# Kernel tuning notes

Measured on AMD Instinct MI355X. Metric: run time of the kernel, lower is better.

## Reference

```python
import jax, jax.numpy as jnp
import numpy as np

NX = 48
NY = 48
K0DX = 0.2026833935483871
N_PML = 8
_PI = 3.1415926


def _fun_s(u):
    # PML stretch factor s(u) = kappa(u) + 1j*sigma_over_omega(u)
    power_kappa = 3
    kappa_max = 15
    power_sigma = 3
    lambda_over_dx = 40
    sigma_over_omega_max = 0.8 * (power_sigma + 1) * lambda_over_dx / (2 * _PI)
    return (1.0 + (kappa_max - 1) * u ** power_kappa) + 1j * (sigma_over_omega_max * u ** power_sigma)


def _lap1d_pml(N, N_L, N_R):
    # 1D second-difference operator with stretched-coordinate PML (dense numpy, constant)
    ddx1 = np.eye(N + 1, N) - np.eye(N + 1, N, k=-1)   # forward difference (N+1, N)
    ddx2 = -ddx1.T                                      # (N, N+1)
    s_half = np.ones(N + 1, dtype=np.complex128)
    s_int = np.ones(N, dtype=np.complex128)
    if N_R > 0:
        s_half[N - N_R:N + 1] = _fun_s(np.arange(0.5, N_R + 1, 1.0) / (N_R + 1))
        s_int[N - N_R:N] = _fun_s(np.arange(1.0, N_R + 1, 1.0) / (N_R + 1))
    if N_L > 0:
        s_half[N_L::-1] = _fun_s(np.arange(0.5, N_L + 1, 1.0) / (N_L + 1))
        s_int[N_L - 1::-1] = _fun_s(np.arange(1.0, N_L + 1, 1.0) / (N_L + 1))
    return np.diag(1.0 / s_int) @ ddx2 @ np.diag(1.0 / s_half) @ ddx1


def _build_A1():
    # 2D Helmholtz Laplacian with PML: kron(Ax, I) + kron(I, Ay), dense 2304x2304 complex64
    Ax = _lap1d_pml(NX, N_PML, N_PML)
    Ay = _lap1d_pml(NY, N_PML, N_PML)
    return (np.kron(Ax, np.eye(NY)) + np.kron(np.eye(NX), Ay)).astype(np.complex64)


_A1 = _build_A1()  # constant system matrix part


def setup_inputs() -> dict:
    key = jax.random.key(0)
    k1, k2, k3, k4, k5 = jax.random.split(key, 5)
    return {
        "n_prediction": jax.random.uniform(k1, (1, NX, NY, 1), dtype=jnp.float32),
        "n_predict_allresults": jax.random.normal(k2, (1, NX, NY, 1), dtype=jnp.float32),
        "x_b": jax.random.normal(k3, (1, NX, NY, 1), dtype=jnp.float32),
        "y_aim": jax.random.normal(k4, (1, NX, NY, 2), dtype=jnp.float32),
        "simulation_region": jax.random.normal(k5, (1, NX, NY, 1), dtype=jnp.float32),
    }


def reference(n_prediction, n_predict_allresults, x_b, y_aim, simulation_region):
    A1 = jnp.asarray(_A1)  # (2304, 2304) complex64
    # A = A1 + k0dx^2 * diag(n^2), with n flattened after [0,2,1,3] transpose
    n_c = n_prediction.astype(jnp.complex64)
    n_flat = jnp.transpose(n_c, (0, 2, 1, 3)).reshape(-1)  # (2304,)
    A = A1 + jnp.diag((K0DX ** 2) * n_flat ** 2)
    # RHS b, same transpose+flatten convention
    b = jnp.transpose(x_b.astype(jnp.complex64), (0, 2, 1, 3)).reshape(NX * NY, 1)
    # Dense complex linear solve A psi = b
    psi = jnp.linalg.solve(A, b).reshape(1, NX, NY, 1)
    psi_tot = jnp.transpose(psi, (0, 2, 1, 3))  # (1, 48, 48, 1) complex64
    y_c = y_aim.astype(jnp.complex64)
    err1 = psi_tot * y_c[:, :, :, 0:1]
    err2 = psi_tot * y_c[:, :, :, 1:2]
    en1 = y_c[:, :, :, 0:1] * y_c[:, :, :, 0:1]
    en2 = y_c[:, :, :, 1:2] * y_c[:, :, :, 1:2]
    return jnp.concatenate([err1, err2, en1, en2], axis=-1)  # (1, 48, 48, 4) complex64
```

## Files before the change

### kernel.cpp

```cpp
#include <hip/hip_runtime.h>


#define NXY 48
#define NN  2304

typedef float2 cplx;
typedef double2 zplx;

__device__ __forceinline__ cplx cmk(float x, float y){ return make_float2(x,y); }
__device__ __forceinline__ cplx cmul(cplx a, cplx b){
    return cmk(fmaf(a.x,b.x,-(a.y*b.y)), fmaf(a.x,b.y, a.y*b.x));
}
__device__ __forceinline__ cplx cadd(cplx a, cplx b){ return cmk(a.x+b.x, a.y+b.y); }
__device__ __forceinline__ cplx csub(cplx a, cplx b){ return cmk(a.x-b.x, a.y-b.y); }
__device__ __forceinline__ cplx cneg(cplx a){ return cmk(-a.x,-a.y); }
__device__ __forceinline__ cplx cfms(cplx c, cplx a, cplx b){
    float re = fmaf(-a.x, b.x, fmaf( a.y, b.y, c.x));
    float im = fmaf(-a.x, b.y, fmaf(-a.y, b.x, c.y));
    return cmk(re, im);
}
__device__ __forceinline__ cplx cfma_(cplx c, cplx a, cplx b){
    float re = fmaf(a.x, b.x, fmaf(-a.y, b.y, c.x));
    float im = fmaf(a.x, b.y, fmaf( a.y, b.x, c.y));
    return cmk(re, im);
}
__device__ __forceinline__ cplx cinv(cplx a){
    float s = 1.0f/fmaf(a.x,a.x, a.y*a.y);
    return cmk(a.x*s, -a.y*s);
}
__device__ __forceinline__ cplx shfl_c(cplx v, int lane){
    return cmk(__shfl(v.x, lane), __shfl(v.y, lane));
}
__device__ __forceinline__ cplx bfly_c(cplx v){
    v.x += __shfl_xor(v.x,1); v.y += __shfl_xor(v.y,1);
    v.x += __shfl_xor(v.x,2); v.y += __shfl_xor(v.y,2);
    v.x += __shfl_xor(v.x,4); v.y += __shfl_xor(v.y,4);
    return v;
}

__device__ __forceinline__ zplx zmul64(zplx a, zplx b){
    return make_double2(a.x*b.x - a.y*b.y, a.x*b.y + a.y*b.x);
}
__device__ __forceinline__ zplx zadd64(zplx a, zplx b){ return make_double2(a.x+b.x, a.y+b.y); }
__device__ __forceinline__ zplx zneg64(zplx a){ return make_double2(-a.x, -a.y); }
__device__ __forceinline__ zplx zinv64(zplx a){
    double s = 1.0/(a.x*a.x + a.y*a.y);
    return make_double2(a.x*s, -a.y*s);
}
__device__ __forceinline__ zplx fun_s(double u){
    const double sig = 0.8*4.0*40.0/(2.0*3.1415926);
    double u3 = u*u*u;
    return make_double2(1.0 + 14.0*u3, sig*u3);
}
__device__ __forceinline__ zplx s_half_at(int j){
    if (j <= 8)  return fun_s((8.5 - (double)j)/9.0);
    if (j >= 40) return fun_s(((double)(j-40) + 0.5)/9.0);
    return make_double2(1.0, 0.0);
}
__device__ __forceinline__ zplx s_int_at(int j){
    if (j <= 7)  return fun_s((8.0 - (double)j)/9.0);
    if (j >= 40) return fun_s(((double)(j-40) + 1.0)/9.0);
    return make_double2(1.0, 0.0);
}

__device__ __forceinline__ void gj48(cplx (&m)[6][6], int lr, int lc){
    #pragma unroll 1
    for (int kr=0; kr<8; ++kr){
        bool prow = (lr==kr), pcol = (lc==kr);
        int rsrc = (kr<<3)|lc;
        int csrc = (lr<<3)|kr;
        int dsrc = (kr<<3)|kr;
        #pragma unroll
        for (int kj=0;kj<6;++kj){
            cplx pv = shfl_c(m[kj][kj], dsrc);
            cplx d  = cinv(pv);
            cplx rs[6], cs[6];
            #pragma unroll
            for (int j=0;j<6;++j) rs[j] = shfl_c(m[kj][j], rsrc);
            #pragma unroll
            for (int i=0;i<6;++i) cs[i] = shfl_c(m[i][kj], csrc);
            cplx rsp[6];
            #pragma unroll
            for (int j=0;j<6;++j) rsp[j] = cmul(d, rs[j]);
            cplx u[6];
            #pragma unroll
            for (int i=0;i<6;++i) u[i] = cs[i];
            if (prow) u[kj] = csub(pv, cmk(1.f,0.f));
            #pragma unroll
            for (int i=0;i<6;++i){
                #pragma unroll
                for (int j=0;j<6;++j) m[i][j] = cfms(m[i][j], u[i], rsp[j]);
            }
            if (pcol){
                #pragma unroll
                for (int i=0;i<6;++i) m[i][kj] = cneg(cmul(d, cs[i]));
                if (prow) m[kj][kj] = d;
            }
        }
    }
}

__global__ __launch_bounds__(128,1) void helm_babe(
    const float* __restrict__ n_pred,
    const float* __restrict__ xb,
    const float* __restrict__ yaim,
    float*       __restrict__ out,
    int                       out_size,
    float2*      __restrict__ wsG)
{
    __shared__ cplx dgv[NXY], lov[NXY], hiv[NXY];
    __shared__ float nk[NN];
    __shared__ float bb[NN];
    __shared__ cplx zv[NN];
    __shared__ cplx Hx[NN];
    __shared__ cplx vv[NXY];

    const int t    = threadIdx.x;
    const int lane = t & 63;
    const int wid  = t >> 6;
    const int lr = lane>>3, lc = lane&7;
    const int r0 = 6*lr, c0v = 6*lc;
    const int diagl = (lc<<3)|lc;
    const double k2 = 0.2026833935483871*0.2026833935483871;

    if (t < NXY){
        int a = t;
        zplx isha  = zinv64(s_half_at(a));
        zplx isha1 = zinv64(s_half_at(a+1));
        zplx isi   = zinv64(s_int_at(a));
        zplx dgd = zneg64(zmul64(isi, zadd64(isha,isha1)));
        zplx lod = zmul64(isi, isha);
        zplx hid = zmul64(isi, isha1);
        dgv[a] = cmk((float)dgd.x,(float)dgd.y);
        lov[a] = cmk((float)lod.x,(float)lod.y);
        hiv[a] = cmk((float)hid.x,(float)hid.y);
    }
    for (int e=t; e<NN; e+=128){
        int i_=e/48, a_=e%48;
        float nv = n_pred[a_*48+i_];
        nk[e] = (float)(k2*(double)nv*(double)nv);
        bb[e] = xb[a_*48+i_];
    }
    __syncthreads();

    const int dir    = (wid==0) ? 1 : -1;
    const int ibeg   = (wid==0) ? 0 : 47;
    const int nsteps = (wid==0) ? 25 : 23;

    cplx g[6][6];
    cplx m[6][6];
    cplx zrow[6];
    #pragma unroll
    for (int i=0;i<6;++i) zrow[i] = cmk(0.f,0.f);

    #pragma unroll 1
    for (int step=0; step<nsteps; ++step){
        int ib = ibeg + dir*step;
        bool full = !(wid==0 && step==24);

        cplx zc[6];
        #pragma unroll
        for (int j=0;j<6;++j) zc[j] = shfl_c(zrow[j], diagl);

        cplx ci = cmk(0.f,0.f), czp = cmk(0.f,0.f);
        if (step>0){
            if (dir>0){ ci = cmul(lov[ib], hiv[ib-1]); czp = lov[ib]; }
            else      { ci = cmul(hiv[ib], lov[ib+1]); czp = hiv[ib]; }
        }
        bool same  = (lc==lr), rightn = (lc==lr+1), leftn = (lc+1==lr);
        cplx p[6];
        #pragma unroll
        for (int i=0;i<6;++i){
            int r = r0+i;
            cplx dgr = dgv[r], lor = lov[r], hir = hiv[r];
            cplx ddi = cadd(cadd(dgv[ib], dgr), cmk(nk[ib*48+r],0.f));
            cplx acc = cmk(0.f,0.f);
            #pragma unroll
            for (int j=0;j<6;++j){
                cplx v = (step>0)? cneg(cmul(ci, g[i][j])) : cmk(0.f,0.f);
                if (same){
                    if (j==i)   v = cadd(v, ddi);
                    if (j==i+1) v = cadd(v, hir);
                    if (j+1==i) v = cadd(v, lor);
                }
                if (rightn && i==5 && j==0) v = cadd(v, hir);
                if (leftn  && i==0 && j==5) v = cadd(v, lor);
                m[i][j] = v;
                if (step>0) acc = cfma_(acc, g[i][j], zc[j]);
            }
            p[i] = acc;
        }
        if (step>0){
            #pragma unroll
            for (int i=0;i<6;++i){
                cplx w = bfly_c(p[i]);
                zrow[i] = cfms(cmk(bb[ib*48+r0+i],0.f), czp, w);
            }
        } else {
            #pragma unroll
            for (int i=0;i<6;++i) zrow[i] = cmk(bb[ib*48+r0+i], 0.f);
        }
        if (lc==0){
            #pragma unroll
            for (int i=0;i<6;++i) zv[ib*48+r0+i] = zrow[i];
        }

        if (full){
            gj48(m, lr, lc);
            if (ib == 25){
                #pragma unroll
                for (int i=0;i<6;++i)
                    #pragma unroll
                    for (int j=0;j<6;++j) Hx[(r0+i)*48 + c0v + j] = m[i][j];
            } else {
                #pragma unroll
                for (int i=0;i<6;++i)
                    #pragma unroll
                    for (int j=0;j<6;++j) wsG[ib*NN + (r0+i)*48 + c0v + j] = m[i][j];
            }
            #pragma unroll
            for (int i=0;i<6;++i)
                #pragma unroll
                for (int j=0;j<6;++j) g[i][j] = m[i][j];
        }
    }

    if (wid==1){
        cplx zc[6];
        #pragma unroll
        for (int j=0;j<6;++j) zc[j] = shfl_c(zrow[j], diagl);
        #pragma unroll
        for (int i=0;i<6;++i){
            cplx acc = cmk(0.f,0.f);
            #pragma unroll
            for (int j=0;j<6;++j) acc = cfma_(acc, m[i][j], zc[j]);
            acc = bfly_c(acc);
            if (lc==0) vv[r0+i] = acc;
        }
    }
    __syncthreads();

    cplx xrow[6];
    if (wid==0){
        cplx cf = cmul(hiv[24], lov[25]);
        #pragma unroll
        for (int i=0;i<6;++i)
            #pragma unroll
            for (int j=0;j<6;++j) m[i][j] = cfms(m[i][j], cf, Hx[(r0+i)*48 + c0v + j]);
        #pragma unroll
        for (int i=0;i<6;++i) zrow[i] = cfms(zrow[i], hiv[24], vv[r0+i]);
        gj48(m, lr, lc);
        cplx zc[6];
        #pragma unroll
        for (int j=0;j<6;++j) zc[j] = shfl_c(zrow[j], diagl);
        #pragma unroll
        for (int i=0;i<6;++i){
            cplx acc = cmk(0.f,0.f);
            #pragma unroll
            for (int j=0;j<6;++j) acc = cfma_(acc, m[i][j], zc[j]);
            xrow[i] = bfly_c(acc);
        }
        if (lc==0){
            #pragma unroll
            for (int i=0;i<6;++i) zv[24*48+r0+i] = xrow[i];
        }
        cplx xc[6], tm[6];
        #pragma unroll
        for (int j=0;j<6;++j) xc[j] = shfl_c(xrow[j], diagl);
        #pragma unroll
        for (int j=0;j<6;++j) tm[j] = cfms(zv[25*48+c0v+j], lov[25], xc[j]);
        #pragma unroll
        for (int i=0;i<6;++i){
            cplx acc = cmk(0.f,0.f);
            #pragma unroll
            for (int j=0;j<6;++j) acc = cfma_(acc, Hx[(r0+i)*48 + c0v + j], tm[j]);
            acc = bfly_c(acc);
            if (lc==0) zv[25*48+r0+i] = acc;
        }
    }
    __syncthreads();

    if (wid==0){
        #pragma unroll 1
        for (int ib=23; ib>=0; --ib){
            cplx xc[6], tm[6];
            #pragma unroll
            for (int j=0;j<6;++j) xc[j] = shfl_c(xrow[j], diagl);
            cplx hiib = hiv[ib];
            #pragma unroll
            for (int j=0;j<6;++j) tm[j] = cfms(zv[ib*48+c0v+j], hiib, xc[j]);
            #pragma unroll
            for (int i=0;i<6;++i){
                cplx acc = cmk(0.f,0.f);
                #pragma unroll
                for (int j=0;j<6;++j){
                    cplx Gv = wsG[ib*NN + (r0+i)*48 + c0v + j];
                    acc = cfma_(acc, Gv, tm[j]);
                }
                xrow[i] = bfly_c(acc);
            }
            if (lc==0){
                #pragma unroll
                for (int i=0;i<6;++i) zv[ib*48+r0+i] = xrow[i];
            }
        }
    } else {
        #pragma unroll
        for (int i=0;i<6;++i) xrow[i] = zv[25*48+r0+i];
        #pragma unroll 1
        for (int ib=26; ib<NXY; ++ib){
            cplx xc[6], tm[6];
            #pragma unroll
            for (int j=0;j<6;++j) xc[j] = shfl_c(xrow[j], diagl);
            cplx loib = lov[ib];
            #pragma unroll
            for (int j=0;j<6;++j) tm[j] = cfms(zv[ib*48+c0v+j], loib, xc[j]);
            #pragma unroll
            for (int i=0;i<6;++i){
                cplx acc = cmk(0.f,0.f);
                #pragma unroll
                for (int j=0;j<6;++j){
                    cplx Gv = wsG[ib*NN + (r0+i)*48 + c0v + j];
                    acc = cfma_(acc, Gv, tm[j]);
                }
                xrow[i] = bfly_c(acc);
            }
            if (lc==0){
                #pragma unroll
                for (int i=0;i<6;++i) zv[ib*48+r0+i] = xrow[i];
            }
        }
    }
    __syncthreads();

    for (int e=t; e<NN; e+=128){
        int alpha=e/48, beta=e%48;
        cplx psi = zv[beta*48+alpha];
        float y0=yaim[2*e], y1=yaim[2*e+1];
        if (out_size == NN*4){
            float4 o = make_float4(psi.x*y0, psi.x*y1, y0*y0, y1*y1);
            *(float4*)(out + 4*e) = o;
        } else {
            float* o = out + 8*e;
            o[0]=psi.x*y0; o[1]=psi.y*y0; o[2]=psi.x*y1; o[3]=psi.y*y1;
            o[4]=y0*y0; o[5]=0.f; o[6]=y1*y1; o[7]=0.f;
        }
    }
}

extern "C" void kernel_launch(void* const* d_in, const int* in_sizes, int n_in,
                              void* d_out, int out_size, void* d_ws, size_t ws_size,
                              hipStream_t stream) {
    const float* n_pred = (const float*)d_in[0];
    const float* xb     = (const float*)d_in[2];
    const float* ya     = (const float*)d_in[3];
    float*  out = (float*)d_out;
    float2* wsG = (float2*)d_ws;

    hipLaunchKernelGGL(helm_babe, dim3(1), dim3(128), 0, stream,
                       n_pred, xb, ya, out, out_size, wsG);
}
```

Baseline: 745.3 us.

## Pipeline Gauss-Jordan pivot broadcast, use packed float2 math and vector workspace I/O

Restructures the in-register Gauss-Jordan inversion so the next pivot's row, column and diagonal are updated first and broadcast by shuffles before the rest of the rank-1 update runs, overlapping shuffle latency with FMA work. The pivot-column fixup is folded into the update by adjusting the rsp entry, which removes the separate pcol pass. Complex arithmetic moves to ext_vector float2 with elementwise FMA so the compiler can emit packed FP32 instructions. Workspace stores and loads of the G blocks become float4 accesses. The reordered elimination adds register pressure and must stay numerically equivalent to the original per-pivot order.

```diff
diff --git a/kernel.cpp b/kernel.cpp
--- a/kernel.cpp
+++ b/kernel.cpp
@@ -4,34 +4,30 @@
 #define NXY 48
 #define NN  2304
 
-typedef float2 cplx;
+typedef float v2 __attribute__((ext_vector_type(2)));
 typedef double2 zplx;
 
-__device__ __forceinline__ cplx cmk(float x, float y){ return make_float2(x,y); }
-__device__ __forceinline__ cplx cmul(cplx a, cplx b){
-    return cmk(fmaf(a.x,b.x,-(a.y*b.y)), fmaf(a.x,b.y, a.y*b.x));
-}
-__device__ __forceinline__ cplx cadd(cplx a, cplx b){ return cmk(a.x+b.x, a.y+b.y); }
-__device__ __forceinline__ cplx csub(cplx a, cplx b){ return cmk(a.x-b.x, a.y-b.y); }
-__device__ __forceinline__ cplx cneg(cplx a){ return cmk(-a.x,-a.y); }
-__device__ __forceinline__ cplx cfms(cplx c, cplx a, cplx b){
-    float re = fmaf(-a.x, b.x, fmaf( a.y, b.y, c.x));
-    float im = fmaf(-a.x, b.y, fmaf(-a.y, b.x, c.y));
-    return cmk(re, im);
-}
-__device__ __forceinline__ cplx cfma_(cplx c, cplx a, cplx b){
-    float re = fmaf(a.x, b.x, fmaf(-a.y, b.y, c.x));
-    float im = fmaf(a.x, b.y, fmaf( a.y, b.x, c.y));
-    return cmk(re, im);
-}
-__device__ __forceinline__ cplx cinv(cplx a){
+__device__ __forceinline__ v2 mk2(float x, float y){ v2 r; r.x=x; r.y=y; return r; }
+__device__ __forceinline__ v2 bcx(v2 a){ return __builtin_shufflevector(a,a,0,0); }
+__device__ __forceinline__ v2 bcy(v2 a){ return __builtin_shufflevector(a,a,1,1); }
+__device__ __forceinline__ v2 jswp(v2 a){ v2 r = __builtin_shufflevector(a,a,1,0); r.x = -r.x; return r; }
+__device__ __forceinline__ v2 cmul(v2 a, v2 b){
+    return __builtin_elementwise_fma(bcx(a), b, bcy(a)*jswp(b));
+}
+__device__ __forceinline__ v2 cfma_(v2 c, v2 a, v2 b){
+    return __builtin_elementwise_fma(bcx(a), b, __builtin_elementwise_fma(bcy(a), jswp(b), c));
+}
+__device__ __forceinline__ v2 cfms(v2 c, v2 a, v2 b){
+    return __builtin_elementwise_fma(-bcx(a), b, __builtin_elementwise_fma(-bcy(a), jswp(b), c));
+}
+__device__ __forceinline__ v2 cinv(v2 a){
     float s = 1.0f/fmaf(a.x,a.x, a.y*a.y);
-    return cmk(a.x*s, -a.y*s);
-}
-__device__ __forceinline__ cplx shfl_c(cplx v, int lane){
-    return cmk(__shfl(v.x, lane), __shfl(v.y, lane));
-}
-__device__ __forceinline__ cplx bfly_c(cplx v){
+    return mk2(a.x*s, -a.y*s);
+}
+__device__ __forceinline__ v2 shfl_c(v2 a, int lane){
+    return mk2(__shfl(a.x, lane), __shfl(a.y, lane));
+}
+__device__ __forceinline__ v2 bfly_c(v2 v){
     v.x += __shfl_xor(v.x,1); v.y += __shfl_xor(v.y,1);
     v.x += __shfl_xor(v.x,2); v.y += __shfl_xor(v.y,2);
     v.x += __shfl_xor(v.x,4); v.y += __shfl_xor(v.y,4);
@@ -63,39 +59,57 @@
     return make_double2(1.0, 0.0);
 }
 
-__device__ __forceinline__ void gj48(cplx (&m)[6][6], int lr, int lc){
+__device__ __forceinline__ void gj48(v2 (&m)[6][6], const int lr, const int lc){
+    v2 pv, rs[6], cs[6];
+    {
+        const int rsrc0 = lc, csrc0 = (lr<<3);
+        pv = shfl_c(m[0][0], 0);
+        #pragma unroll
+        for (int j=0;j<6;++j) rs[j] = shfl_c(m[0][j], rsrc0);
+        #pragma unroll
+        for (int i=0;i<6;++i) cs[i] = shfl_c(m[i][0], csrc0);
+    }
     #pragma unroll 1
     for (int kr=0; kr<8; ++kr){
-        bool prow = (lr==kr), pcol = (lc==kr);
-        int rsrc = (kr<<3)|lc;
-        int csrc = (lr<<3)|kr;
-        int dsrc = (kr<<3)|kr;
-        #pragma unroll
-        for (int kj=0;kj<6;++kj){
-            cplx pv = shfl_c(m[kj][kj], dsrc);
-            cplx d  = cinv(pv);
-            cplx rs[6], cs[6];
-            #pragma unroll
-            for (int j=0;j<6;++j) rs[j] = shfl_c(m[kj][j], rsrc);
-            #pragma unroll
-            for (int i=0;i<6;++i) cs[i] = shfl_c(m[i][kj], csrc);
-            cplx rsp[6];
+        const bool prow = (lr==kr), pcol = (lc==kr);
+        #pragma unroll
+        for (int kj=0; kj<6; ++kj){
+            const int nj = (kj+1)%6;
+            const int cr = (kj==5) ? ((kr<7)?(kr+1):7) : kr;
+            const int nrsrc = (cr<<3)|lc;
+            const int ncsrc = (lr<<3)|cr;
+            const int ndsrc = (cr<<3)|cr;
+            v2 d = cinv(pv);
+            v2 rsp[6];
             #pragma unroll
             for (int j=0;j<6;++j) rsp[j] = cmul(d, rs[j]);
-            cplx u[6];
+            if (pcol) rsp[kj] = d + mk2(1.f,0.f);
+            v2 u[6];
             #pragma unroll
             for (int i=0;i<6;++i) u[i] = cs[i];
-            if (prow) u[kj] = csub(pv, cmk(1.f,0.f));
+            if (prow) u[kj] = pv - mk2(1.f,0.f);
+            #pragma unroll
+            for (int j=0;j<6;++j) m[nj][j] = cfms(m[nj][j], u[nj], rsp[j]);
+            #pragma unroll
+            for (int i=0;i<6;++i){ if (i!=nj) m[i][nj] = cfms(m[i][nj], u[i], rsp[nj]); }
+            v2 npv = shfl_c(m[nj][nj], ndsrc);
+            v2 nrs[6], ncs[6];
+            #pragma unroll
+            for (int j=0;j<6;++j) nrs[j] = shfl_c(m[nj][j], nrsrc);
+            #pragma unroll
+            for (int i=0;i<6;++i) ncs[i] = shfl_c(m[i][nj], ncsrc);
             #pragma unroll
             for (int i=0;i<6;++i){
-                #pragma unroll
-                for (int j=0;j<6;++j) m[i][j] = cfms(m[i][j], u[i], rsp[j]);
-            }
-            if (pcol){
-                #pragma unroll
-                for (int i=0;i<6;++i) m[i][kj] = cneg(cmul(d, cs[i]));
-                if (prow) m[kj][kj] = d;
-            }
+                if (i==nj) continue;
+                #pragma unroll
+                for (int j=0;j<6;++j){
+                    if (j==nj) continue;
+                    m[i][j] = cfms(m[i][j], u[i], rsp[j]);
+                }
+            }
+            pv = npv;
+            #pragma unroll
+            for (int j=0;j<6;++j){ rs[j]=nrs[j]; cs[j]=ncs[j]; }
         }
     }
 }
@@ -106,14 +120,14 @@
     const float* __restrict__ yaim,
     float*       __restrict__ out,
     int                       out_size,
-    float2*      __restrict__ wsG)
+    float*       __restrict__ wsG)
 {
-    __shared__ cplx dgv[NXY], lov[NXY], hiv[NXY];
+    __shared__ v2 dgv[NXY], lov[NXY], hiv[NXY];
     __shared__ float nk[NN];
     __shared__ float bb[NN];
-    __shared__ cplx zv[NN];
-    __shared__ cplx Hx[NN];
-    __shared__ cplx vv[NXY];
+    __shared__ v2 zv[NN];
+    __shared__ v2 Hx[NN];
+    __shared__ v2 vv[NXY];
 
     const int t    = threadIdx.x;
     const int lane = t & 63;
@@ -131,9 +145,9 @@
         zplx dgd = zneg64(zmul64(isi, zadd64(isha,isha1)));
         zplx lod = zmul64(isi, isha);
         zplx hid = zmul64(isi, isha1);
-        dgv[a] = cmk((float)dgd.x,(float)dgd.y);
-        lov[a] = cmk((float)lod.x,(float)lod.y);
-        hiv[a] = cmk((float)hid.x,(float)hid.y);
+        dgv[a] = mk2((float)dgd.x,(float)dgd.y);
+        lov[a] = mk2((float)lod.x,(float)lod.y);
+        hiv[a] = mk2((float)hid.x,(float)hid.y);
     }
     for (int e=t; e<NN; e+=128){
         int i_=e/48, a_=e%48;
@@ -147,44 +161,45 @@
     const int ibeg   = (wid==0) ? 0 : 47;
     const int nsteps = (wid==0) ? 25 : 23;
 
-    cplx g[6][6];
-    cplx m[6][6];
-    cplx zrow[6];
+    v2 g[6][6];
+    v2 m[6][6];
+    v2 zrow[6];
     #pragma unroll
-    for (int i=0;i<6;++i) zrow[i] = cmk(0.f,0.f);
+    for (int i=0;i<6;++i) zrow[i] = mk2(0.f,0.f);
 
     #pragma unroll 1
     for (int step=0; step<nsteps; ++step){
         int ib = ibeg + dir*step;
         bool full = !(wid==0 && step==24);
 
-        cplx zc[6];
+        v2 zc[6];
         #pragma unroll
         for (int j=0;j<6;++j) zc[j] = shfl_c(zrow[j], diagl);
 
-        cplx ci = cmk(0.f,0.f), czp = cmk(0.f,0.f);
+        v2 nci = mk2(0.f,0.f), czp = mk2(0.f,0.f);
         if (step>0){
-            if (dir>0){ ci = cmul(lov[ib], hiv[ib-1]); czp = lov[ib]; }
-            else      { ci = cmul(hiv[ib], lov[ib+1]); czp = hiv[ib]; }
+            if (dir>0){ nci = cmul(lov[ib], hiv[ib-1]); czp = lov[ib]; }
+            else      { nci = cmul(hiv[ib], lov[ib+1]); czp = hiv[ib]; }
+            nci = -nci;
         }
         bool same  = (lc==lr), rightn = (lc==lr+1), leftn = (lc+1==lr);
-        cplx p[6];
+        v2 p[6];
         #pragma unroll
         for (int i=0;i<6;++i){
             int r = r0+i;
-            cplx dgr = dgv[r], lor = lov[r], hir = hiv[r];
-            cplx ddi = cadd(cadd(dgv[ib], dgr), cmk(nk[ib*48+r],0.f));
-            cplx acc = cmk(0.f,0.f);
+            v2 dgr = dgv[r], lor = lov[r], hir = hiv[r];
+            v2 ddi = dgv[ib] + dgr + mk2(nk[ib*48+r],0.f);
+            v2 acc = mk2(0.f,0.f);
             #pragma unroll
             for (int j=0;j<6;++j){
-                cplx v = (step>0)? cneg(cmul(ci, g[i][j])) : cmk(0.f,0.f);
+                v2 v = (step>0)? cmul(nci, g[i][j]) : mk2(0.f,0.f);
                 if (same){
-                    if (j==i)   v = cadd(v, ddi);
-                    if (j==i+1) v = cadd(v, hir);
-                    if (j+1==i) v = cadd(v, lor);
-                }
-                if (rightn && i==5 && j==0) v = cadd(v, hir);
-                if (leftn  && i==0 && j==5) v = cadd(v, lor);
+                    if (j==i)   v = v + ddi;
+                    if (j==i+1) v = v + hir;
+                    if (j+1==i) v = v + lor;
+                }
+                if (rightn && i==5 && j==0) v = v + hir;
+                if (leftn  && i==0 && j==5) v = v + lor;
                 m[i][j] = v;
                 if (step>0) acc = cfma_(acc, g[i][j], zc[j]);
             }
@@ -193,12 +208,12 @@
         if (step>0){
             #pragma unroll
             for (int i=0;i<6;++i){
-                cplx w = bfly_c(p[i]);
-                zrow[i] = cfms(cmk(bb[ib*48+r0+i],0.f), czp, w);
+                v2 w = bfly_c(p[i]);
+                zrow[i] = cfms(mk2(bb[ib*48+r0+i],0.f), czp, w);
             }
         } else {
             #pragma unroll
-            for (int i=0;i<6;++i) zrow[i] = cmk(bb[ib*48+r0+i], 0.f);
+            for (int i=0;i<6;++i) zrow[i] = mk2(bb[ib*48+r0+i], 0.f);
         }
         if (lc==0){
             #pragma unroll
@@ -214,9 +229,16 @@
                     for (int j=0;j<6;++j) Hx[(r0+i)*48 + c0v + j] = m[i][j];
             } else {
                 #pragma unroll
-                for (int i=0;i<6;++i)
+                for (int i=0;i<6;++i){
+                    float4* w4 = (float4*)(wsG + 2*((size_t)ib*NN + (r0+i)*48 + c0v));
                     #pragma unroll
-                    for (int j=0;j<6;++j) wsG[ib*NN + (r0+i)*48 + c0v + j] = m[i][j];
+                    for (int jp=0;jp<3;++jp){
+                        float4 f;
+                        f.x = m[i][2*jp].x;   f.y = m[i][2*jp].y;
+                        f.z = m[i][2*jp+1].x; f.w = m[i][2*jp+1].y;
+                        w4[jp] = f;
+                    }
+                }
             }
             #pragma unroll
             for (int i=0;i<6;++i)
@@ -226,12 +248,12 @@
     }
 
     if (wid==1){
-        cplx zc[6];
+        v2 zc[6];
         #pragma unroll
         for (int j=0;j<6;++j) zc[j] = shfl_c(zrow[j], diagl);
         #pragma unroll
         for (int i=0;i<6;++i){
-            cplx acc = cmk(0.f,0.f);
+            v2 acc = mk2(0.f,0.f);
             #pragma unroll
             for (int j=0;j<6;++j) acc = cfma_(acc, m[i][j], zc[j]);
             acc = bfly_c(acc);
@@ -240,9 +262,9 @@
     }
     __syncthreads();
 
-    cplx xrow[6];
+    v2 xrow[6];
     if (wid==0){
-        cplx cf = cmul(hiv[24], lov[25]);
+        v2 cf = cmul(hiv[24], lov[25]);
         #pragma unroll
         for (int i=0;i<6;++i)
             #pragma unroll
@@ -250,12 +272,12 @@
         #pragma unroll
         for (int i=0;i<6;++i) zrow[i] = cfms(zrow[i], hiv[24], vv[r0+i]);
         gj48(m, lr, lc);
-        cplx zc[6];
+        v2 zc[6];
         #pragma unroll
         for (int j=0;j<6;++j) zc[j] = shfl_c(zrow[j], diagl);
         #pragma unroll
         for (int i=0;i<6;++i){
-            cplx acc = cmk(0.f,0.f);
+            v2 acc = mk2(0.f,0.f);
             #pragma unroll
             for (int j=0;j<6;++j) acc = cfma_(acc, m[i][j], zc[j]);
             xrow[i] = bfly_c(acc);
@@ -264,14 +286,14 @@
             #pragma unroll
             for (int i=0;i<6;++i) zv[24*48+r0+i] = xrow[i];
         }
-        cplx xc[6], tm[6];
+        v2 xc[6], tm[6];
         #pragma unroll
         for (int j=0;j<6;++j) xc[j] = shfl_c(xrow[j], diagl);
         #pragma unroll
         for (int j=0;j<6;++j) tm[j] = cfms(zv[25*48+c0v+j], lov[25], xc[j]);
         #pragma unroll
         for (int i=0;i<6;++i){
-            cplx acc = cmk(0.f,0.f);
+            v2 acc = mk2(0.f,0.f);
             #pragma unroll
             for (int j=0;j<6;++j) acc = cfma_(acc, Hx[(r0+i)*48 + c0v + j], tm[j]);
             acc = bfly_c(acc);
@@ -283,19 +305,21 @@
     if (wid==0){
         #pragma unroll 1
         for (int ib=23; ib>=0; --ib){
-            cplx xc[6], tm[6];
+            v2 xc[6], tm[6];
             #pragma unroll
             for (int j=0;j<6;++j) xc[j] = shfl_c(xrow[j], diagl);
-            cplx hiib = hiv[ib];
+            v2 hiib = hiv[ib];
             #pragma unroll
             for (int j=0;j<6;++j) tm[j] = cfms(zv[ib*48+c0v+j], hiib, xc[j]);
             #pragma unroll
             for (int i=0;i<6;++i){
-                cplx acc = cmk(0.f,0.f);
-                #pragma unroll
-                for (int j=0;j<6;++j){
-                    cplx Gv = wsG[ib*NN + (r0+i)*48 + c0v + j];
-                    acc = cfma_(acc, Gv, tm[j]);
+                const float4* w4 = (const float4*)(wsG + 2*((size_t)ib*NN + (r0+i)*48 + c0v));
+                v2 acc = mk2(0.f,0.f);
+                #pragma unroll
+                for (int jp=0;jp<3;++jp){
+                    float4 f = w4[jp];
+                    acc = cfma_(acc, mk2(f.x,f.y), tm[2*jp]);
+                    acc = cfma_(acc, mk2(f.z,f.w), tm[2*jp+1]);
                 }
                 xrow[i] = bfly_c(acc);
             }
@@ -309,19 +333,21 @@
         for (int i=0;i<6;++i) xrow[i] = zv[25*48+r0+i];
         #pragma unroll 1
         for (int ib=26; ib<NXY; ++ib){
-            cplx xc[6], tm[6];
+            v2 xc[6], tm[6];
             #pragma unroll
             for (int j=0;j<6;++j) xc[j] = shfl_c(xrow[j], diagl);
-            cplx loib = lov[ib];
+            v2 loib = lov[ib];
             #pragma unroll
             for (int j=0;j<6;++j) tm[j] = cfms(zv[ib*48+c0v+j], loib, xc[j]);
             #pragma unroll
             for (int i=0;i<6;++i){
-                cplx acc = cmk(0.f,0.f);
-                #pragma unroll
-                for (int j=0;j<6;++j){
-                    cplx Gv = wsG[ib*NN + (r0+i)*48 + c0v + j];
-                    acc = cfma_(acc, Gv, tm[j]);
+                const float4* w4 = (const float4*)(wsG + 2*((size_t)ib*NN + (r0+i)*48 + c0v));
+                v2 acc = mk2(0.f,0.f);
+                #pragma unroll
+                for (int jp=0;jp<3;++jp){
+                    float4 f = w4[jp];
+                    acc = cfma_(acc, mk2(f.x,f.y), tm[2*jp]);
+                    acc = cfma_(acc, mk2(f.z,f.w), tm[2*jp+1]);
                 }
                 xrow[i] = bfly_c(acc);
             }
@@ -335,7 +361,7 @@
 
     for (int e=t; e<NN; e+=128){
         int alpha=e/48, beta=e%48;
-        cplx psi = zv[beta*48+alpha];
+        v2 psi = zv[beta*48+alpha];
         float y0=yaim[2*e], y1=yaim[2*e+1];
         if (out_size == NN*4){
             float4 o = make_float4(psi.x*y0, psi.x*y1, y0*y0, y1*y1);
@@ -354,8 +380,8 @@
     const float* n_pred = (const float*)d_in[0];
     const float* xb     = (const float*)d_in[2];
     const float* ya     = (const float*)d_in[3];
-    float*  out = (float*)d_out;
-    float2* wsG = (float2*)d_ws;
+    float* out = (float*)d_out;
+    float* wsG = (float*)d_ws;
 
     hipLaunchKernelGGL(helm_babe, dim3(1), dim3(128), 0, stream,
                        n_pred, xb, ya, out, out_size, wsG);
```

New measurement: 615.5 us. 1.21x faster.
